# Kernel optimization log

Hardware: AMD Instinct MI355X
Metric: run time of the kernel (lower is better)

The kernel has to match this reference:

```python
import jax, jax.numpy as jnp
import numpy as np

HIDDEN = 1024
N_HEADS = 16
HEAD_DIM = HIDDEN // N_HEADS  # 64; RoPE applied only to first HEAD_DIM channels (head 0)
NUM_BUCKETS = 32
MAX_DISTANCE = 128
MLP_HIDDEN = 4 * HIDDEN
B, N = 2, 2048


def _rotate_half(x):
    # interleaved pairs [a0,b0,a1,b1,...] -> [-b0,a0,-b1,a1,...]
    sh = x.shape
    xr = x.reshape(sh[:-1] + (sh[-1] // 2, 2))
    x1, x2 = xr[..., 0], xr[..., 1]
    return jnp.stack([-x2, x1], axis=-1).reshape(sh)


def _rel_bucket(n, num_buckets=NUM_BUCKETS, max_distance=MAX_DISTANCE):
    # bidirectional T5 bucketing
    ctx = jnp.arange(n)[:, None]
    mem = jnp.arange(n)[None, :]
    rp = mem - ctx  # [n, n]
    nb = num_buckets // 2
    buckets = jnp.where(rp > 0, nb, 0)
    rp = jnp.abs(rp)
    max_exact = nb // 2
    is_small = rp < max_exact
    log_ratio = jnp.log(jnp.maximum(rp, 1).astype(jnp.float32) / max_exact)
    rpl = max_exact + (log_ratio / np.log(max_distance / max_exact) * (nb - max_exact)).astype(jnp.int32)
    rpl = jnp.minimum(rpl, nb - 1)
    return buckets + jnp.where(is_small, rp, rpl)


def _ln(x, eps=1e-6):
    # LayerNorm without affine (DiT elementwise_affine=False)
    m = jnp.mean(x, axis=-1, keepdims=True)
    v = jnp.mean(jnp.square(x - m), axis=-1, keepdims=True)
    return (x - m) * jax.lax.rsqrt(v + eps)


def setup_inputs() -> dict:
    key = jax.random.key(0)
    ks = jax.random.split(key, 12)
    s = 0.02
    return {
        "x": jax.random.normal(ks[0], (B, N, HIDDEN), dtype=jnp.float32),
        "c": jax.random.normal(ks[1], (B, HIDDEN), dtype=jnp.float32),
        "w_ada": jax.random.normal(ks[2], (HIDDEN, 6 * HIDDEN), dtype=jnp.float32) * s,
        "b_ada": jnp.zeros((6 * HIDDEN,), dtype=jnp.float32),
        "w_qkv": jax.random.normal(ks[3], (HIDDEN, 3 * HIDDEN), dtype=jnp.float32) * s,
        "b_qkv": jnp.zeros((3 * HIDDEN,), dtype=jnp.float32),
        "w_out": jax.random.normal(ks[4], (HIDDEN, HIDDEN), dtype=jnp.float32) * s,
        "b_out": jnp.zeros((HIDDEN,), dtype=jnp.float32),
        "rel_table": jax.random.normal(ks[5], (NUM_BUCKETS, N_HEADS), dtype=jnp.float32) * s,
        "w_mlp1": jax.random.normal(ks[6], (HIDDEN, MLP_HIDDEN), dtype=jnp.float32) * s,
        "b_mlp1": jnp.zeros((MLP_HIDDEN,), dtype=jnp.float32),
        "w_mlp2": jax.random.normal(ks[7], (MLP_HIDDEN, HIDDEN), dtype=jnp.float32) * s,
        "b_mlp2": jnp.zeros((HIDDEN,), dtype=jnp.float32),
    }


def reference(x, c, w_ada, b_ada, w_qkv, b_qkv, w_out, b_out, rel_table,
              w_mlp1, b_mlp1, w_mlp2, b_mlp2):
    Bb, n, hid = x.shape
    hd = HEAD_DIM

    # AdaLN-Zero modulation params from conditioning
    mod = jax.nn.silu(c) @ w_ada + b_ada  # [B, 6*hid]
    sh_msa, sc_msa, g_msa, sh_mlp, sc_mlp, g_mlp = jnp.split(mod, 6, axis=-1)

    # --- attention branch ---
    h = _ln(x) * (1.0 + sc_msa[:, None, :]) + sh_msa[:, None, :]
    qkv = h @ w_qkv + b_qkv
    q, k, v = jnp.split(qkv, 3, axis=-1)  # each [B, N, hid]

    # partial RoPE: only first head_dim channels (head 0), interleaved-duplicated freqs
    t = jnp.arange(n, dtype=jnp.float32)
    inv_freq = 1.0 / (10000.0 ** (jnp.arange(0, hd, 2, dtype=jnp.float32) / hd))
    fr = t[:, None] * inv_freq[None, :]               # [N, hd/2]
    fr = jnp.stack([fr, fr], axis=-1).reshape(n, hd)  # [N, hd] interleaved dup
    cos, sin = jnp.cos(fr)[None], jnp.sin(fr)[None]

    def partial_rope(a):
        r, u = a[..., :hd], a[..., hd:]
        r = r * cos + _rotate_half(r) * sin
        return jnp.concatenate([r, u], axis=-1)

    q = partial_rope(q)
    k = partial_rope(k)

    qh = q.reshape(Bb, n, N_HEADS, hd)
    kh = k.reshape(Bb, n, N_HEADS, hd)
    vh = v.reshape(Bb, n, N_HEADS, hd)

    scores = jnp.einsum('bqhd,bkhd->bhqk', qh, kh) / np.float32(np.sqrt(hd))
    bias = rel_table[_rel_bucket(n)]                 # [N, N, H]
    scores = scores + jnp.transpose(bias, (2, 0, 1))[None]  # [1,H,N,N]
    attn = jax.nn.softmax(scores, axis=-1)
    ctxv = jnp.einsum('bhqk,bkhd->bqhd', attn, vh).reshape(Bb, n, hid)
    attn_out = ctxv @ w_out + b_out
    x = x + g_msa[:, None, :] * attn_out

    # --- MLP branch ---
    h2 = _ln(x) * (1.0 + sc_mlp[:, None, :]) + sh_mlp[:, None, :]
    m = jax.nn.gelu(h2 @ w_mlp1 + b_mlp1, approximate=True) @ w_mlp2 + b_mlp2
    return x + g_mlp[:, None, :] * m
```

## Files before the change

### kernel.cpp

```cpp
#include <hip/hip_runtime.h>
#include <hip/hip_bf16.h>

#define SEQ 2048

typedef float f32x4 __attribute__((ext_vector_type(4)));
typedef float f32x16 __attribute__((ext_vector_type(16)));
typedef short short8 __attribute__((ext_vector_type(8)));
typedef int int4v __attribute__((ext_vector_type(4)));

static __device__ __forceinline__ unsigned short f2bf(float f) {
  __hip_bfloat16 h = __float2bfloat16(f);
  unsigned short u;
  __builtin_memcpy(&u, &h, 2);
  return u;
}
static __device__ __forceinline__ float bf2f(unsigned short u) {
  __hip_bfloat16 h;
  __builtin_memcpy(&h, &u, 2);
  return __bfloat162float(h);
}
static __device__ __forceinline__ void gload16(const void* g, void* l) {
  __builtin_amdgcn_global_load_lds(
      (const __attribute__((address_space(1))) void*)g,
      (__attribute__((address_space(3))) void*)l, 16, 0, 0);
}
static __device__ __forceinline__ float gelu_t(float x) {
  float t = x * x;
  float z = x * fmaf(0.1029442695044937f, t, 2.3021181827964594f);
  return x * __builtin_amdgcn_rcpf(1.f + exp2f(-z));
}
static __device__ __forceinline__ unsigned int cvtpk(float lo, float hi) {
  unsigned int r;
  asm("v_cvt_pk_bf16_f32 %0, %1, %2" : "=v"(r) : "v"(lo), "v"(hi));
  return r;
}


__global__ void silu_k(const float* __restrict__ c, float* __restrict__ o) {
  int i = blockIdx.x * 256 + threadIdx.x;
  float v = c[i];
  o[i] = v / (1.f + expf(-v));
}

__global__ void mod_part_k(const float* __restrict__ siluc, const float* __restrict__ w_ada,
                           float* __restrict__ part) {
  int gid = blockIdx.x * 256 + threadIdx.x;
  int kc = gid / 12288;
  int idx = gid - kc * 12288;
  int b = idx / 6144;
  int j = idx - b * 6144;
  const float* cp = siluc + b * 1024 + kc * 64;
  const float* wp = w_ada + (size_t)kc * 64 * 6144 + j;
  float acc = 0.f;
#pragma unroll 8
  for (int k = 0; k < 64; ++k) acc += cp[k] * wp[(size_t)k * 6144];
  part[gid] = acc;
}

__global__ void mod_reduce_k(const float* __restrict__ part, const float* __restrict__ b_ada,
                             float* __restrict__ mod) {
  int idx = blockIdx.x * 256 + threadIdx.x;
  int j = idx % 6144;
  float a = b_ada[j];
#pragma unroll
  for (int kc = 0; kc < 16; ++kc) a += part[kc * 12288 + idx];
  mod[idx] = a;
}

__global__ void brp_k(const float* __restrict__ rel_table, float* __restrict__ brp) {
  int idx = blockIdx.x * 256 + threadIdx.x;
  int h = idx >> 12, pos = idx & 4095;
  int rp = pos - 2047;
  int bucket = rp > 0 ? 16 : 0;
  int a = rp < 0 ? -rp : rp;
  int bi;
  if (a < 8) {
    bi = a;
  } else {
    bi = 8 + (int)(logf((float)a / 8.f) / 2.772588722239781f * 8.f);
    if (bi > 15) bi = 15;
  }
  brp[idx] = rel_table[(bucket + bi) * 16 + h] * 1.4426950408889634f;
}

__global__ void transpose_cvt(const float* __restrict__ src, unsigned short* __restrict__ dst,
                              int K, int N) {
  __shared__ float tile[32][33];
  int nt = blockIdx.x, kt = blockIdx.y;
  int t = threadIdx.x;
  int col = t & 31, r0 = t >> 5;
#pragma unroll
  for (int i = 0; i < 4; ++i) {
    int r = r0 + i * 8;
    tile[r][col] = src[(size_t)(kt * 32 + r) * N + nt * 32 + col];
  }
  __syncthreads();
#pragma unroll
  for (int i = 0; i < 4; ++i) {
    int r = r0 + i * 8;
    dst[(size_t)(nt * 32 + r) * K + kt * 32 + col] = f2bf(tile[col][r]);
  }
}

__global__ void ln_mod(const float* __restrict__ x, const float* __restrict__ mod,
                       unsigned short* __restrict__ out, int sh_off, int sc_off) {
  int row = blockIdx.x;
  int b = row >> 11;
  int t = threadIdx.x;
  const float4 v = ((const float4*)(x + (size_t)row * 1024))[t];
  float s1 = v.x + v.y + v.z + v.w;
  float s2 = v.x * v.x + v.y * v.y + v.z * v.z + v.w * v.w;
#pragma unroll
  for (int off = 32; off; off >>= 1) {
    s1 += __shfl_xor(s1, off);
    s2 += __shfl_xor(s2, off);
  }
  __shared__ float red[8];
  int w = t >> 6, lane = t & 63;
  if (lane == 0) { red[w] = s1; red[4 + w] = s2; }
  __syncthreads();
  s1 = red[0] + red[1] + red[2] + red[3];
  s2 = red[4] + red[5] + red[6] + red[7];
  float mean = s1 * (1.f / 1024.f);
  float var = s2 * (1.f / 1024.f) - mean * mean;
  float rstd = rsqrtf(var + 1e-6f);
  const float* mb = mod + (size_t)b * 6144;
  int col = t * 4;
  ushort4 o4;
  o4.x = f2bf((v.x - mean) * rstd * (1.f + mb[sc_off + col + 0]) + mb[sh_off + col + 0]);
  o4.y = f2bf((v.y - mean) * rstd * (1.f + mb[sc_off + col + 1]) + mb[sh_off + col + 1]);
  o4.z = f2bf((v.z - mean) * rstd * (1.f + mb[sc_off + col + 2]) + mb[sh_off + col + 2]);
  o4.w = f2bf((v.w - mean) * rstd * (1.f + mb[sc_off + col + 3]) + mb[sh_off + col + 3]);
  *((ushort4*)(out + (size_t)row * 1024 + col)) = o4;
}

__global__ void rope_k(unsigned short* __restrict__ qkv) {
  int t = threadIdx.x;
  int row = blockIdx.x * 4 + (t >> 6);
  int sub = t & 63;
  int which = sub >> 5;
  int i = sub & 31;
  int n = row & (SEQ - 1);
  size_t base = (size_t)row * 3072 + which * 1024 + 2 * i;
  float x0 = bf2f(qkv[base]), x1 = bf2f(qkv[base + 1]);
  float freq = exp2f(-(float)(2 * i) * (13.287712379549449f / 64.f));
  float ang = (float)n * freq;
  float s = sinf(ang), co = cosf(ang);
  qkv[base] = f2bf(x0 * co - x1 * s);
  qkv[base + 1] = f2bf(x1 * co + x0 * s);
}

__global__ void kvpack(const unsigned short* __restrict__ qkv, unsigned short* __restrict__ kpk,
                       unsigned short* __restrict__ vpk) {
  const int kt = blockIdx.x;
  const int bh = blockIdx.y;
  const int b = bh >> 4, h = bh & 15;
  const int t = threadIdx.x;
  const int s = t >> 6, lane = t & 63;
  const int l31 = lane & 31, hi = lane >> 5;
  const size_t outbase = ((size_t)(bh * 64 + kt) * 4 + s) * 512 + lane * 8;
  {
    const unsigned short* src =
        qkv + (size_t)(b * SEQ + kt * 32 + l31) * 3072 + 1024 + h * 64 + s * 16 + hi * 8;
    *(short8*)(kpk + outbase) = *(const short8*)src;
  }
  {
    const int krow = kt * 32 + (s & 1) * 16 + hi * 8;
    const int d = (s >> 1) * 32 + l31;
    const unsigned short* src = qkv + (size_t)(b * SEQ + krow) * 3072 + 2048 + h * 64 + d;
    unsigned short v[8];
#pragma unroll
    for (int j = 0; j < 8; ++j) v[j] = src[(size_t)j * 3072];
    *(short8*)(vpk + outbase) = *(const short8*)v;
  }
}

template <int MODE, int BN>
__global__ __launch_bounds__(256) void gemm_bt(
    const unsigned short* __restrict__ A, const unsigned short* __restrict__ Bt,
    const float* __restrict__ bias, void* __restrict__ outp, const float* __restrict__ res,
    const float* __restrict__ mod, int goff, int N, int K) {
  __shared__ __align__(16) unsigned short a_lds[128 * 64];
  __shared__ __align__(16) unsigned short b_lds[BN * 64];
  constexpr int MT = (BN == 128) ? 4 : 2;
  const int t = threadIdx.x;
  const int lane = t & 63;
  const int l15 = lane & 15, l4 = lane >> 4;
  const int w = t >> 6;
  const int wr = (BN == 128) ? (w >> 1) : w;
  const int wc = (BN == 128) ? (w & 1) : 0;
  constexpr int WROWS = (BN == 128) ? 64 : 32;
  const int rowA0 = blockIdx.y * 128;
  const int rowB0 = blockIdx.x * BN;
  const int wub = t & ~63;

  f32x4 acc[MT][4];
#pragma unroll
  for (int m = 0; m < MT; ++m)
#pragma unroll
    for (int n = 0; n < 4; ++n) acc[m][n] = (f32x4){0.f, 0.f, 0.f, 0.f};

  for (int kt = 0; kt < K; kt += 64) {
#pragma unroll
    for (int rnd = 0; rnd < 4; ++rnd) {
      const int idx = rnd * 256 + t;
      const int row = idx >> 3;
      const int cb = ((idx & 7) << 4) ^ ((row & 7) << 4);
      const char* sa = (const char*)(A + (size_t)(rowA0 + row) * K + kt) + cb;
      gload16(sa, (char*)a_lds + (size_t)(rnd * 256 + wub) * 16);
    }
#pragma unroll
    for (int rnd = 0; rnd < BN / 32; ++rnd) {
      const int idx = rnd * 256 + t;
      const int row = idx >> 3;
      const int cb = ((idx & 7) << 4) ^ ((row & 7) << 4);
      const char* sb = (const char*)(Bt + (size_t)(rowB0 + row) * K + kt) + cb;
      gload16(sb, (char*)b_lds + (size_t)(rnd * 256 + wub) * 16);
    }
    __syncthreads();
#pragma unroll
    for (int kb = 0; kb < 2; ++kb) {
      short8 af[MT], bfr[4];
#pragma unroll
      for (int m = 0; m < MT; ++m) {
        int row = wr * WROWS + m * 16 + l15;
        int cb = (kb * 64 + l4 * 16) ^ ((row & 7) << 4);
        af[m] = *(const short8*)((const char*)a_lds + row * 128 + cb);
      }
#pragma unroll
      for (int n = 0; n < 4; ++n) {
        int row = wc * 64 + n * 16 + l15;
        int cb = (kb * 64 + l4 * 16) ^ ((row & 7) << 4);
        bfr[n] = *(const short8*)((const char*)b_lds + row * 128 + cb);
      }
      __builtin_amdgcn_s_setprio(1);
#pragma unroll
      for (int m = 0; m < MT; ++m)
#pragma unroll
        for (int n = 0; n < 4; ++n)
          acc[m][n] = __builtin_amdgcn_mfma_f32_16x16x32_bf16(af[m], bfr[n], acc[m][n], 0, 0, 0);
      __builtin_amdgcn_s_setprio(0);
    }
    __syncthreads();
  }

#pragma unroll
  for (int n = 0; n < 4; ++n) {
    const int col = rowB0 + wc * 64 + n * 16 + l15;
    const float bv = bias[col];
#pragma unroll
    for (int m = 0; m < MT; ++m) {
      const int row0 = rowA0 + wr * WROWS + m * 16 + l4 * 4;
#pragma unroll
      for (int r = 0; r < 4; ++r) {
        float v = acc[m][n][r] + bv;
        const size_t o = (size_t)(row0 + r) * N + col;
        if (MODE == 0) {
          ((unsigned short*)outp)[o] = f2bf(v);
        } else if (MODE == 1) {
          ((unsigned short*)outp)[o] = f2bf(gelu_t(v));
        } else {
          float g = mod[(size_t)((row0 + r) >> 11) * 6144 + goff + col];
          ((float*)outp)[o] = res[o] + g * v;
        }
      }
    }
  }
}

__global__ __launch_bounds__(256) void attn_k(const unsigned short* __restrict__ qkv,
                                              const unsigned short* __restrict__ kpk,
                                              const unsigned short* __restrict__ vpk,
                                              const float* __restrict__ brp_all,
                                              unsigned short* __restrict__ ctxv) {
  const int t = threadIdx.x;
  const int w = t >> 6;
  const int lane = t & 63;
  const int l31 = lane & 31;
  const int hi = lane >> 5;
  const int wg = blockIdx.x;
  const int xcd = wg & 7, idx = wg >> 3;
  const int bh = xcd * 4 + (idx >> 4);
  const int qt = idx & 15;
  const int b = bh >> 4, h = bh & 15;
  const int qw = qt * 128 + w * 32;
  const float SC = 0.125f * 1.4426950408889634f;
  const float* brp = brp_all + (size_t)h * 4096;

  short8 qfr[4];
  {
    const unsigned short* qrow = qkv + (size_t)(b * SEQ + qw + l31) * 3072 + h * 64 + hi * 8;
#pragma unroll
    for (int kk = 0; kk < 4; ++kk) qfr[kk] = *(const short8*)(qrow + kk * 16);
  }
  const float bfar_pos = brp[4095], bfar_neg = brp[0];
  const float* bql = brp + 2047 + 4 * hi - (qw + l31);

  const unsigned short* kp = kpk + (size_t)(bh * 64) * 2048 + lane * 8;
  const unsigned short* vp = vpk + (size_t)(bh * 64) * 2048 + lane * 8;

  short8 kfrA[4], vfrA[4], kfrB[4], vfrB[4];
#pragma unroll
  for (int s = 0; s < 4; ++s) {
    kfrA[s] = *(const short8*)(kp + s * 512);
    vfrA[s] = *(const short8*)(vp + s * 512);
  }
  kp += 2048;
  vp += 2048;

  f32x16 oacc0 = {}, oacc1 = {};
  float mrow = -1e30f, lsum = 0.f;
  int kbase = 0;

#define ATTN_TILE(KF, VF, KFN, VFN)                                                       \
  do {                                                                                    \
               \
    KFN[0] = *(const short8*)(kp);                                                        \
    KFN[1] = *(const short8*)(kp + 512);                                                  \
    KFN[2] = *(const short8*)(kp + 1024);                                                 \
    KFN[3] = *(const short8*)(kp + 1536);                                                 \
    VFN[0] = *(const short8*)(vp);                                                        \
    VFN[1] = *(const short8*)(vp + 512);                                                  \
    VFN[2] = *(const short8*)(vp + 1024);                                                 \
    VFN[3] = *(const short8*)(vp + 1536);                                                 \
    kp += 2048;                                                                           \
    vp += 2048;                                                                           \
    f32x16 sacc = {};                                                                     \
    sacc = __builtin_amdgcn_mfma_f32_32x32x16_bf16(KF[0], qfr[0], sacc, 0, 0, 0);         \
    sacc = __builtin_amdgcn_mfma_f32_32x32x16_bf16(KF[1], qfr[1], sacc, 0, 0, 0);         \
    sacc = __builtin_amdgcn_mfma_f32_32x32x16_bf16(KF[2], qfr[2], sacc, 0, 0, 0);         \
    sacc = __builtin_amdgcn_mfma_f32_32x32x16_bf16(KF[3], qfr[3], sacc, 0, 0, 0);         \
    float sv[16];                                                                         \
    const int dd = kbase - qw;                                                            \
    if (dd >= 128 || dd <= -128) {                                                        \
      const float bf_ = (dd > 0) ? bfar_pos : bfar_neg;                                   \
      _Pragma("unroll") for (int r = 0; r < 16; ++r) sv[r] = fmaf(sacc[r], SC, bf_);      \
    } else {                                                                              \
      const float* bp = bql + kbase;                                                      \
      _Pragma("unroll") for (int r = 0; r < 16; ++r)                                      \
          sv[r] = fmaf(sacc[r], SC, bp[(r & 3) + 8 * (r >> 2)]);                          \
    }                                                                                     \
    float a0 = fmaxf(sv[0], sv[1]), a1 = fmaxf(sv[2], sv[3]);                             \
    float a2 = fmaxf(sv[4], sv[5]), a3 = fmaxf(sv[6], sv[7]);                             \
    float a4 = fmaxf(sv[8], sv[9]), a5 = fmaxf(sv[10], sv[11]);                           \
    float a6 = fmaxf(sv[12], sv[13]), a7 = fmaxf(sv[14], sv[15]);                         \
    float b0 = fmaxf(fmaxf(a0, a1), fmaxf(a2, a3));                                       \
    float b1 = fmaxf(fmaxf(a4, a5), fmaxf(a6, a7));                                       \
    float mh = fmaxf(b0, b1);                                                             \
    const float mx = fmaxf(mh, __shfl_xor(mh, 32));                                       \
    if (__any(mx > mrow + 8.f)) {                                                         \
      float mn = fmaxf(mrow, mx);                                                         \
      float scl = __builtin_amdgcn_exp2f(mrow - mn);                                      \
      mrow = mn;                                                                          \
      lsum *= scl;                                                                        \
      _Pragma("unroll") for (int r = 0; r < 16; ++r) {                                    \
        oacc0[r] *= scl;                                                                  \
        oacc1[r] *= scl;                                                                  \
      }                                                                                   \
    }                                                                                     \
    float p[16];                                                                          \
    _Pragma("unroll") for (int r = 0; r < 16; ++r)                                        \
        p[r] = __builtin_amdgcn_exp2f(sv[r] - mrow);                                      \
    lsum += (((p[0] + p[1]) + (p[2] + p[3])) + ((p[4] + p[5]) + (p[6] + p[7]))) +         \
            (((p[8] + p[9]) + (p[10] + p[11])) + ((p[12] + p[13]) + (p[14] + p[15])));    \
    unsigned int x0 = cvtpk(p[0], p[1]), x1 = cvtpk(p[2], p[3]);                          \
    unsigned int y0 = cvtpk(p[4], p[5]), y1 = cvtpk(p[6], p[7]);                          \
    asm("v_permlane32_swap_b32 %0, %1" : "+v"(x0), "+v"(y0));                             \
    asm("v_permlane32_swap_b32 %0, %1" : "+v"(x1), "+v"(y1));                             \
    unsigned int x2 = cvtpk(p[8], p[9]), x3 = cvtpk(p[10], p[11]);                        \
    unsigned int y2 = cvtpk(p[12], p[13]), y3 = cvtpk(p[14], p[15]);                      \
    asm("v_permlane32_swap_b32 %0, %1" : "+v"(x2), "+v"(y2));                             \
    asm("v_permlane32_swap_b32 %0, %1" : "+v"(x3), "+v"(y3));                             \
    int4v pi0 = {(int)x0, (int)x1, (int)y0, (int)y1};                                     \
    int4v pi1 = {(int)x2, (int)x3, (int)y2, (int)y3};                                     \
    short8 pf0 = __builtin_bit_cast(short8, pi0);                                         \
    short8 pf1 = __builtin_bit_cast(short8, pi1);                                         \
    oacc0 = __builtin_amdgcn_mfma_f32_32x32x16_bf16(VF[0], pf0, oacc0, 0, 0, 0);          \
    oacc0 = __builtin_amdgcn_mfma_f32_32x32x16_bf16(VF[1], pf1, oacc0, 0, 0, 0);          \
    oacc1 = __builtin_amdgcn_mfma_f32_32x32x16_bf16(VF[2], pf0, oacc1, 0, 0, 0);          \
    oacc1 = __builtin_amdgcn_mfma_f32_32x32x16_bf16(VF[3], pf1, oacc1, 0, 0, 0);          \
    kbase += 32;                                                                          \
  } while (0)

#pragma unroll 1
  for (int it = 0; it < 32; ++it) {
    ATTN_TILE(kfrA, vfrA, kfrB, vfrB);
    ATTN_TILE(kfrB, vfrB, kfrA, vfrA);
  }
#undef ATTN_TILE

  const float ltot = lsum + __shfl_xor(lsum, 32);
  const float inv = 1.f / ltot;

  unsigned short* orow = ctxv + (size_t)(b * SEQ + qw + l31) * 1024 + h * 64;
#pragma unroll
  for (int r = 0; r < 16; r += 2) {
    const int d = (r & 3) + 8 * (r >> 2) + 4 * hi;
    *(unsigned int*)(orow + d) = cvtpk(oacc0[r] * inv, oacc0[r + 1] * inv);
    *(unsigned int*)(orow + 32 + d) = cvtpk(oacc1[r] * inv, oacc1[r + 1] * inv);
  }
}

extern "C" void kernel_launch(void* const* d_in, const int* in_sizes, int n_in, void* d_out,
                              int out_size, void* d_ws, size_t ws_size, hipStream_t stream) {
  (void)in_sizes; (void)n_in; (void)out_size; (void)ws_size;
  const float* x = (const float*)d_in[0];
  const float* c = (const float*)d_in[1];
  const float* w_ada = (const float*)d_in[2];
  const float* b_ada = (const float*)d_in[3];
  const float* w_qkv = (const float*)d_in[4];
  const float* b_qkv = (const float*)d_in[5];
  const float* w_out = (const float*)d_in[6];
  const float* b_out = (const float*)d_in[7];
  const float* rel_t = (const float*)d_in[8];
  const float* w_mlp1 = (const float*)d_in[9];
  const float* b_mlp1 = (const float*)d_in[10];
  const float* w_mlp2 = (const float*)d_in[11];
  const float* b_mlp2 = (const float*)d_in[12];
  float* out = (float*)d_out;
  char* ws = (char*)d_ws;

  constexpr size_t OFF_WQKVT = 0;
  constexpr size_t OFF_WOUTT = OFF_WQKVT + (size_t)3072 * 1024 * 2;
  constexpr size_t OFF_WM1T = OFF_WOUTT + (size_t)1024 * 1024 * 2;
  constexpr size_t OFF_WM2T = OFF_WM1T + (size_t)4096 * 1024 * 2;
  constexpr size_t OFF_H = OFF_WM2T + (size_t)1024 * 4096 * 2;
  constexpr size_t OFF_QKV = OFF_H + (size_t)4096 * 1024 * 2;
  constexpr size_t OFF_VT = OFF_QKV + (size_t)4096 * 3072 * 2;
  constexpr size_t OFF_CTXV = OFF_VT + (size_t)32 * 64 * 2048 * 2;
  constexpr size_t OFF_MID = OFF_CTXV + (size_t)4096 * 1024 * 2;
  constexpr size_t OFF_SILU = OFF_MID + (size_t)4096 * 4096 * 2;
  constexpr size_t OFF_MOD = OFF_SILU + 2048 * 4;
  constexpr size_t OFF_BRP = OFF_MOD + 12288 * 4;
  constexpr size_t OFF_PART = OFF_BRP + 65536 * 4;

  unsigned short* wqkvT = (unsigned short*)(ws + OFF_WQKVT);
  unsigned short* woutT = (unsigned short*)(ws + OFF_WOUTT);
  unsigned short* wm1T = (unsigned short*)(ws + OFF_WM1T);
  unsigned short* wm2T = (unsigned short*)(ws + OFF_WM2T);
  unsigned short* hbuf = (unsigned short*)(ws + OFF_H);
  unsigned short* qkvbuf = (unsigned short*)(ws + OFF_QKV);
  unsigned short* vpkbuf = (unsigned short*)(ws + OFF_VT);
  unsigned short* ctxvbuf = (unsigned short*)(ws + OFF_CTXV);
  unsigned short* midbuf = (unsigned short*)(ws + OFF_MID);
  unsigned short* kpkbuf = (unsigned short*)(ws + OFF_MID);
  float* siluc = (float*)(ws + OFF_SILU);
  float* modb = (float*)(ws + OFF_MOD);
  float* brp = (float*)(ws + OFF_BRP);
  float* part = (float*)(ws + OFF_PART);

  silu_k<<<8, 256, 0, stream>>>(c, siluc);
  mod_part_k<<<768, 256, 0, stream>>>(siluc, w_ada, part);
  mod_reduce_k<<<48, 256, 0, stream>>>(part, b_ada, modb);
  transpose_cvt<<<dim3(96, 32), 256, 0, stream>>>(w_qkv, wqkvT, 1024, 3072);
  transpose_cvt<<<dim3(32, 32), 256, 0, stream>>>(w_out, woutT, 1024, 1024);
  transpose_cvt<<<dim3(128, 32), 256, 0, stream>>>(w_mlp1, wm1T, 1024, 4096);
  transpose_cvt<<<dim3(32, 128), 256, 0, stream>>>(w_mlp2, wm2T, 4096, 1024);
  brp_k<<<256, 256, 0, stream>>>(rel_t, brp);

  ln_mod<<<4096, 256, 0, stream>>>(x, modb, hbuf, 0, 1024);
  gemm_bt<0, 128><<<dim3(24, 32), 256, 0, stream>>>(hbuf, wqkvT, b_qkv, qkvbuf, nullptr, nullptr,
                                                    0, 3072, 1024);
  rope_k<<<1024, 256, 0, stream>>>(qkvbuf);
  kvpack<<<dim3(64, 32), 256, 0, stream>>>(qkvbuf, kpkbuf, vpkbuf);
  attn_k<<<512, 256, 0, stream>>>(qkvbuf, kpkbuf, vpkbuf, brp, ctxvbuf);
  gemm_bt<2, 64><<<dim3(16, 32), 256, 0, stream>>>(ctxvbuf, woutT, b_out, out, x, modb, 2048,
                                                   1024, 1024);
  ln_mod<<<4096, 256, 0, stream>>>(out, modb, hbuf, 3072, 4096);
  gemm_bt<1, 128><<<dim3(32, 32), 256, 0, stream>>>(hbuf, wm1T, b_mlp1, midbuf, nullptr, nullptr,
                                                    0, 4096, 1024);
  gemm_bt<2, 64><<<dim3(16, 32), 256, 0, stream>>>(midbuf, wm2T, b_mlp2, out, out, modb, 5120,
                                                   1024, 4096);
}
```

Before: 285.4 us.

## Add XCD-aware block remapping and 64x64 tiles for N=1024 GEMMs

The GEMM kernel now takes the M tile size as a template parameter and uses a fixed 2x2 wave layout. The two N=1024 projections (attention output and MLP down) move from 128x64 to 64x64 tiles, doubling their grid to 1024 blocks for better CU fill. All GEMMs also remap block IDs round-robin across the eight chiplets, aiming to keep neighbouring tiles on the same XCD and improve L2 reuse. The smaller tiles give less operand reuse per block, and the remap assumes the block count is divisible by eight.

```diff
diff --git a/kernel.cpp b/kernel.cpp
--- a/kernel.cpp
+++ b/kernel.cpp
@@ -175,34 +175,39 @@
   }
 }
 
-template <int MODE, int BN>
+template <int MODE, int BM, int BN>
 __global__ __launch_bounds__(256) void gemm_bt(
     const unsigned short* __restrict__ A, const unsigned short* __restrict__ Bt,
     const float* __restrict__ bias, void* __restrict__ outp, const float* __restrict__ res,
     const float* __restrict__ mod, int goff, int N, int K) {
-  __shared__ __align__(16) unsigned short a_lds[128 * 64];
+  __shared__ __align__(16) unsigned short a_lds[BM * 64];
   __shared__ __align__(16) unsigned short b_lds[BN * 64];
-  constexpr int MT = (BN == 128) ? 4 : 2;
+  constexpr int WAVES_N = 2, WAVES_M = 2;
+  constexpr int WM = BM / WAVES_M, WN = BN / WAVES_N;
+  constexpr int MT = WM / 16, NT = WN / 16;
   const int t = threadIdx.x;
   const int lane = t & 63;
   const int l15 = lane & 15, l4 = lane >> 4;
   const int w = t >> 6;
-  const int wr = (BN == 128) ? (w >> 1) : w;
-  const int wc = (BN == 128) ? (w & 1) : 0;
-  constexpr int WROWS = (BN == 128) ? 64 : 32;
-  const int rowA0 = blockIdx.y * 128;
-  const int rowB0 = blockIdx.x * BN;
+  const int wr = w >> 1, wc = w & 1;
+  const int gx = gridDim.x;
+  const int nwg = gx * gridDim.y;
+  int wg = blockIdx.y * gx + blockIdx.x;
+  wg = (wg & 7) * (nwg >> 3) + (wg >> 3);
+  const int by = wg / gx, bx = wg - by * gx;
+  const int rowA0 = by * BM;
+  const int rowB0 = bx * BN;
   const int wub = t & ~63;
 
-  f32x4 acc[MT][4];
+  f32x4 acc[MT][NT];
 #pragma unroll
   for (int m = 0; m < MT; ++m)
 #pragma unroll
-    for (int n = 0; n < 4; ++n) acc[m][n] = (f32x4){0.f, 0.f, 0.f, 0.f};
+    for (int n = 0; n < NT; ++n) acc[m][n] = (f32x4){0.f, 0.f, 0.f, 0.f};
 
   for (int kt = 0; kt < K; kt += 64) {
 #pragma unroll
-    for (int rnd = 0; rnd < 4; ++rnd) {
+    for (int rnd = 0; rnd < BM / 32; ++rnd) {
       const int idx = rnd * 256 + t;
       const int row = idx >> 3;
       const int cb = ((idx & 7) << 4) ^ ((row & 7) << 4);
@@ -220,16 +225,16 @@
     __syncthreads();
 #pragma unroll
     for (int kb = 0; kb < 2; ++kb) {
-      short8 af[MT], bfr[4];
+      short8 af[MT], bfr[NT];
 #pragma unroll
       for (int m = 0; m < MT; ++m) {
-        int row = wr * WROWS + m * 16 + l15;
+        int row = wr * WM + m * 16 + l15;
         int cb = (kb * 64 + l4 * 16) ^ ((row & 7) << 4);
         af[m] = *(const short8*)((const char*)a_lds + row * 128 + cb);
       }
 #pragma unroll
-      for (int n = 0; n < 4; ++n) {
-        int row = wc * 64 + n * 16 + l15;
+      for (int n = 0; n < NT; ++n) {
+        int row = wc * WN + n * 16 + l15;
         int cb = (kb * 64 + l4 * 16) ^ ((row & 7) << 4);
         bfr[n] = *(const short8*)((const char*)b_lds + row * 128 + cb);
       }
@@ -237,7 +242,7 @@
 #pragma unroll
       for (int m = 0; m < MT; ++m)
 #pragma unroll
-        for (int n = 0; n < 4; ++n)
+        for (int n = 0; n < NT; ++n)
           acc[m][n] = __builtin_amdgcn_mfma_f32_16x16x32_bf16(af[m], bfr[n], acc[m][n], 0, 0, 0);
       __builtin_amdgcn_s_setprio(0);
     }
@@ -245,12 +250,12 @@
   }
 
 #pragma unroll
-  for (int n = 0; n < 4; ++n) {
-    const int col = rowB0 + wc * 64 + n * 16 + l15;
+  for (int n = 0; n < NT; ++n) {
+    const int col = rowB0 + wc * WN + n * 16 + l15;
     const float bv = bias[col];
 #pragma unroll
     for (int m = 0; m < MT; ++m) {
-      const int row0 = rowA0 + wr * WROWS + m * 16 + l4 * 4;
+      const int row0 = rowA0 + wr * WM + m * 16 + l4 * 4;
 #pragma unroll
       for (int r = 0; r < 4; ++r) {
         float v = acc[m][n][r] + bv;
@@ -459,16 +464,16 @@
   brp_k<<<256, 256, 0, stream>>>(rel_t, brp);
 
   ln_mod<<<4096, 256, 0, stream>>>(x, modb, hbuf, 0, 1024);
-  gemm_bt<0, 128><<<dim3(24, 32), 256, 0, stream>>>(hbuf, wqkvT, b_qkv, qkvbuf, nullptr, nullptr,
-                                                    0, 3072, 1024);
+  gemm_bt<0, 128, 128><<<dim3(24, 32), 256, 0, stream>>>(hbuf, wqkvT, b_qkv, qkvbuf, nullptr,
+                                                         nullptr, 0, 3072, 1024);
   rope_k<<<1024, 256, 0, stream>>>(qkvbuf);
   kvpack<<<dim3(64, 32), 256, 0, stream>>>(qkvbuf, kpkbuf, vpkbuf);
   attn_k<<<512, 256, 0, stream>>>(qkvbuf, kpkbuf, vpkbuf, brp, ctxvbuf);
-  gemm_bt<2, 64><<<dim3(16, 32), 256, 0, stream>>>(ctxvbuf, woutT, b_out, out, x, modb, 2048,
-                                                   1024, 1024);
+  gemm_bt<2, 64, 64><<<dim3(16, 64), 256, 0, stream>>>(ctxvbuf, woutT, b_out, out, x, modb, 2048,
+                                                       1024, 1024);
   ln_mod<<<4096, 256, 0, stream>>>(out, modb, hbuf, 3072, 4096);
-  gemm_bt<1, 128><<<dim3(32, 32), 256, 0, stream>>>(hbuf, wm1T, b_mlp1, midbuf, nullptr, nullptr,
-                                                    0, 4096, 1024);
-  gemm_bt<2, 64><<<dim3(16, 32), 256, 0, stream>>>(midbuf, wm2T, b_mlp2, out, out, modb, 5120,
-                                                   1024, 4096);
-}
+  gemm_bt<1, 128, 128><<<dim3(32, 32), 256, 0, stream>>>(hbuf, wm1T, b_mlp1, midbuf, nullptr,
+                                                         nullptr, 0, 4096, 1024);
+  gemm_bt<2, 64, 64><<<dim3(16, 64), 256, 0, stream>>>(midbuf, wm2T, b_mlp2, out, out, modb, 5120,
+                                                       1024, 4096);
+}
```

Result: faster. 273.6 us (-4.1%).
